# Optimization experiments

Hardware: AMD Instinct MI355X
Metric: run time of the kernel (lower is better)

## Reference

```python
import jax, jax.numpy as jnp
import numpy as np

DIM = 192
SCALE = DIM ** (-0.5)


def setup_inputs() -> dict:
    key = jax.random.key(0)
    qkv = jax.random.normal(key, (8, 4096, 3 * DIM), dtype=jnp.float32)
    return {"qkv": qkv}


def reference(qkv):
    # qkv: [B, T, 3C] -> q, k, v each [B, T, C]
    q, k, v = jnp.split(qkv, 3, axis=2)
    # scale_in=True: scale q and k before distance computation
    q = q * SCALE
    k = k * SCALE
    # L2-distance attention logits: -||q_t - k_s||_2, computed via the
    # expansion ||q||^2 + ||k||^2 - 2 q.k (same as torch.cdist for large inputs)
    q2 = jnp.sum(q * q, axis=-1)          # [B, T]
    k2 = jnp.sum(k * k, axis=-1)          # [B, S]
    d2 = q2[:, :, None] + k2[:, None, :] - 2.0 * jnp.einsum('btc,bsc->bts', q, k)
    d2 = jnp.maximum(d2, 0.0)
    # safe sqrt (zero distance on the diagonal since q and k come from same tokens)
    dist = jnp.where(d2 > 0, jnp.sqrt(jnp.where(d2 > 0, d2, 1.0)), 0.0)
    attn_logits = -dist                    # [B, T, S]
    attn = jax.nn.softmax(attn_logits, axis=-1)
    return jnp.einsum('bts,bsc->btc', attn, v)  # [B, T, C]
```

## Files before the change

### kernel.cpp

```cpp
#include <hip/hip_runtime.h>
#include <hip/hip_bf16.h>


#define BB 8
#define TT 4096
#define CD 192

typedef __attribute__((ext_vector_type(8))) short short8;
typedef __attribute__((ext_vector_type(4))) float float4v;
typedef __attribute__((ext_vector_type(2))) unsigned int uint2v;

constexpr float A2C = (float)(2.0813689810056077 / 192.0);

static __device__ __forceinline__ unsigned short f2bf(float f) {
  unsigned u = __builtin_bit_cast(unsigned, f);
  unsigned r = u + 0x7fffu + ((u >> 16) & 1u);
  return (unsigned short)(r >> 16);
}
static __device__ __forceinline__ float bf2f(unsigned short b) {
  return __builtin_bit_cast(float, (unsigned)b << 16);
}

__global__ __launch_bounds__(256) void prep(
    const float* __restrict__ qkv, short8* __restrict__ qsw,
    short8* __restrict__ ksw, short8* __restrict__ vsw,
    float* __restrict__ q2, float* __restrict__ k2) {
  __shared__ unsigned short tile[32 * 584];
  const int t = threadIdx.x;
  const int b = blockIdx.x >> 7;
  const int sc = blockIdx.x & 127;
  const float* src = qkv + ((size_t)(b * TT + sc * 32)) * (3 * CD);
#pragma unroll
  for (int j = 0; j < 18; ++j) {
    int f = j * 256 + t;
    int row = f / 144, c4 = (f % 144) * 4;
    float4v x = *(const float4v*)(src + (size_t)row * 576 + c4);
    unsigned r0 = (unsigned)f2bf(x[0]) | ((unsigned)f2bf(x[1]) << 16);
    unsigned r1 = (unsigned)f2bf(x[2]) | ((unsigned)f2bf(x[3]) << 16);
    *(uint2v*)&tile[row * 584 + c4] = (uint2v){r0, r1};
  }
  __syncthreads();

  const int lane = t & 63, w = t >> 6;
  const int L = lane & 15, q = lane >> 4;
  const int which = w >> 1;
  const int s16o = w & 1;
  const int row = s16o * 16 + L;
  short8* dst = which ? ksw : qsw;
  const size_t ubase = ((size_t)(b * 256 + sc * 2 + s16o)) * 6;
  float ss = 0.f;
#pragma unroll
  for (int ch = 0; ch < 6; ++ch) {
    short8 fr = *(const short8*)&tile[row * 584 + which * CD + ch * 32 + q * 8];
#pragma unroll
    for (int j = 0; j < 8; ++j) {
      float f = bf2f((unsigned short)fr[j]);
      ss += f * f;
    }
    dst[(ubase + ch) * 64 + lane] = fr;
  }
  ss += __shfl_xor(ss, 16);
  ss += __shfl_xor(ss, 32);
  if (lane < 16)
    (which ? k2 : q2)[b * TT + sc * 32 + s16o * 16 + lane] = ss;

#pragma unroll
  for (int i = 0; i < 3; ++i) {
    int nt2 = w * 3 + i;
    short8 fr;
#pragma unroll
    for (int j = 0; j < 8; ++j)
      fr[j] = (short)tile[(q * 8 + j) * 584 + 2 * CD + nt2 * 16 + L];
    vsw[((size_t)(b * 12 + nt2) * 128 + sc) * 64 + lane] = fr;
  }
}

__global__ __launch_bounds__(256, 1) void attn2(
    const short8* __restrict__ qsw, const short8* __restrict__ ksw,
    const short8* __restrict__ vsw, const float* __restrict__ q2,
    const float* __restrict__ k2, float* __restrict__ out) {
  __shared__ __align__(16) unsigned char s_lds[49152 + 9216];
  float* ldsP = (float*)(s_lds + 49152);

  const int tid = threadIdx.x;
  const int w = tid >> 6;
  const int lane = tid & 63;
  const int L = lane & 15;
  const int q = lane >> 4;
  const int b = blockIdx.x & 7;
  const int qt = blockIdx.x >> 3;
  const int q0 = qt * 128 + w * 32;
  const size_t bT = (size_t)b * TT;

  float* pw = ldsP + w * 576;

  auto stage = [&](int itile, int buf) {
    const char* gk = (const char*)(ksw + ((size_t)(b * 256 + 2 * itile)) * 6 * 64);
#pragma unroll
    for (int j = 0; j < 3; ++j) {
      int u = w * 3 + j;
      const char* ga = gk + (u * 64 + lane) * 16;
      char* la = (char*)s_lds + buf * 12288 + u * 1024;
      __builtin_amdgcn_global_load_lds(
          (const __attribute__((address_space(1))) void*)ga,
          (__attribute__((address_space(3))) void*)la, 16, 0, 0);
    }
#pragma unroll
    for (int j = 0; j < 3; ++j) {
      int u = w * 3 + j;
      const char* ga = (const char*)vsw +
                       (((size_t)(b * 12 + u) * 128 + itile) * 64 + lane) * 16;
      char* la = (char*)s_lds + 24576 + buf * 12288 + u * 1024;
      __builtin_amdgcn_global_load_lds(
          (const __attribute__((address_space(1))) void*)ga,
          (__attribute__((address_space(3))) void*)la, 16, 0, 0);
    }
  };

  short8 qf[2][6];
#pragma unroll
  for (int mt = 0; mt < 2; ++mt)
#pragma unroll
    for (int ch = 0; ch < 6; ++ch)
      qf[mt][ch] = qsw[((size_t)(b * 256 + (q0 >> 4) + mt) * 6 + ch) * 64 + lane];

  float q2l[2][4];
#pragma unroll
  for (int mt = 0; mt < 2; ++mt)
#pragma unroll
    for (int r = 0; r < 4; ++r)
      q2l[mt][r] = q2[bT + q0 + mt * 16 + 4 * q + r];

  float4v oacc[2][12];
#pragma unroll
  for (int mt = 0; mt < 2; ++mt)
#pragma unroll
    for (int nt = 0; nt < 12; ++nt) oacc[mt][nt] = (float4v){0.f, 0.f, 0.f, 0.f};
  float lsum[2][4] = {{0.f, 0.f, 0.f, 0.f}, {0.f, 0.f, 0.f, 0.f}};

  stage(0, 0);
  __syncthreads();

#pragma unroll 1
  for (int it = 0; it < 128; ++it) {
    const int cur = it & 1;
    if (it + 1 < 128) stage(it + 1, cur ^ 1);
    const int s0 = it * 32;

    float k2l[2];
    k2l[0] = k2[bT + s0 + L];
    k2l[1] = k2[bT + s0 + 16 + L];

    float4v sacc[2][2];
#pragma unroll
    for (int mt = 0; mt < 2; ++mt)
#pragma unroll
      for (int nt = 0; nt < 2; ++nt) sacc[mt][nt] = (float4v){0.f, 0.f, 0.f, 0.f};
#pragma unroll
    for (int ch = 0; ch < 6; ++ch) {
      short8 kf0 = *(const short8*)(s_lds + cur * 12288 + ch * 1024 + lane * 16);
      short8 kf1 = *(const short8*)(s_lds + cur * 12288 + (6 + ch) * 1024 + lane * 16);
      sacc[0][0] = __builtin_amdgcn_mfma_f32_16x16x32_bf16(qf[0][ch], kf0, sacc[0][0], 0, 0, 0);
      sacc[1][0] = __builtin_amdgcn_mfma_f32_16x16x32_bf16(qf[1][ch], kf0, sacc[1][0], 0, 0, 0);
      sacc[0][1] = __builtin_amdgcn_mfma_f32_16x16x32_bf16(qf[0][ch], kf1, sacc[0][1], 0, 0, 0);
      sacc[1][1] = __builtin_amdgcn_mfma_f32_16x16x32_bf16(qf[1][ch], kf1, sacc[1][1], 0, 0, 0);
    }

    short8 vf[12];
#pragma unroll
    for (int nt = 0; nt < 12; ++nt)
      vf[nt] = *(const short8*)(s_lds + 24576 + cur * 12288 + nt * 1024 + lane * 16);

    short8 paf[2];
#pragma unroll
    for (int mt = 0; mt < 2; ++mt) {
#pragma unroll
      for (int nt = 0; nt < 2; ++nt)
#pragma unroll
        for (int r = 0; r < 4; ++r) {
          float dot = sacc[mt][nt][r];
          float tt = fmaf(-2.f, dot, q2l[mt][r] + k2l[nt]);
          float y = fmaxf(tt, 0.f) * A2C;
          float p = __builtin_amdgcn_exp2f(-__builtin_amdgcn_sqrtf(y));
          lsum[mt][r] += p;
          pw[(4 * q + r) * 36 + nt * 16 + L] = p;
        }
      float4v p0 = *(const float4v*)(pw + L * 36 + q * 8);
      float4v p1 = *(const float4v*)(pw + L * 36 + q * 8 + 4);
      short8 pa;
#pragma unroll
      for (int j = 0; j < 4; ++j) {
        pa[j] = (short)f2bf(p0[j]);
        pa[j + 4] = (short)f2bf(p1[j]);
      }
      paf[mt] = pa;
    }

#pragma unroll
    for (int nt = 0; nt < 12; ++nt) {
      oacc[0][nt] = __builtin_amdgcn_mfma_f32_16x16x32_bf16(paf[0], vf[nt], oacc[0][nt], 0, 0, 0);
      oacc[1][nt] = __builtin_amdgcn_mfma_f32_16x16x32_bf16(paf[1], vf[nt], oacc[1][nt], 0, 0, 0);
    }

    __syncthreads();
  }

#pragma unroll
  for (int mt = 0; mt < 2; ++mt)
#pragma unroll
    for (int r = 0; r < 4; ++r) {
      float ls = lsum[mt][r];
#pragma unroll
      for (int m = 1; m < 16; m <<= 1) ls += __shfl_xor(ls, m);
      float linv = 1.f / ls;
#pragma unroll
      for (int nt = 0; nt < 12; ++nt)
        out[(bT + q0 + mt * 16 + 4 * q + r) * CD + nt * 16 + L] =
            oacc[mt][nt][r] * linv;
    }
}

extern "C" void kernel_launch(void* const* d_in, const int* in_sizes, int n_in,
                              void* d_out, int out_size, void* d_ws, size_t ws_size,
                              hipStream_t stream) {
  (void)in_sizes; (void)n_in; (void)out_size; (void)ws_size;
  const float* qkv = (const float*)d_in[0];
  float* out = (float*)d_out;

  short8* qsw = (short8*)d_ws;
  short8* ksw = qsw + (size_t)BB * 256 * 6 * 64;
  short8* vsw = ksw + (size_t)BB * 256 * 6 * 64;
  float* q2 = (float*)(vsw + (size_t)BB * 12 * 128 * 64);
  float* k2 = q2 + (size_t)BB * TT;

  prep<<<BB * 128, 256, 0, stream>>>(qkv, qsw, ksw, vsw, q2, k2);
  attn2<<<BB * 32, 256, 0, stream>>>(qsw, ksw, vsw, q2, k2, out);
}
```

Before: 303.9 us.

## Halve per-wave query rows and double grid to raise occupancy

Measured after the change: 244.3 us. -19.6%, faster.

```diff
diff --git a/kernel.cpp b/kernel.cpp
--- a/kernel.cpp
+++ b/kernel.cpp
@@ -62,7 +62,7 @@
   ss += __shfl_xor(ss, 16);
   ss += __shfl_xor(ss, 32);
   if (lane < 16)
-    (which ? k2 : q2)[b * TT + sc * 32 + s16o * 16 + lane] = ss;
+    (which ? k2 : q2)[b * TT + sc * 32 + s16o * 16 + lane] = ss * A2C;
 
 #pragma unroll
   for (int i = 0; i < 3; ++i) {
@@ -75,7 +75,7 @@
   }
 }
 
-__global__ __launch_bounds__(256, 1) void attn2(
+__global__ __launch_bounds__(256, 2) void attn2(
     const short8* __restrict__ qsw, const short8* __restrict__ ksw,
     const short8* __restrict__ vsw, const float* __restrict__ q2,
     const float* __restrict__ k2, float* __restrict__ out) {
@@ -89,7 +89,7 @@
   const int q = lane >> 4;
   const int b = blockIdx.x & 7;
   const int qt = blockIdx.x >> 3;
-  const int q0 = qt * 128 + w * 32;
+  const int q0 = qt * 64 + w * 16;
   const size_t bT = (size_t)b * TT;
 
   float* pw = ldsP + w * 576;
@@ -117,26 +117,19 @@
     }
   };
 
-  short8 qf[2][6];
-#pragma unroll
-  for (int mt = 0; mt < 2; ++mt)
-#pragma unroll
-    for (int ch = 0; ch < 6; ++ch)
-      qf[mt][ch] = qsw[((size_t)(b * 256 + (q0 >> 4) + mt) * 6 + ch) * 64 + lane];
-
-  float q2l[2][4];
-#pragma unroll
-  for (int mt = 0; mt < 2; ++mt)
-#pragma unroll
-    for (int r = 0; r < 4; ++r)
-      q2l[mt][r] = q2[bT + q0 + mt * 16 + 4 * q + r];
-
-  float4v oacc[2][12];
-#pragma unroll
-  for (int mt = 0; mt < 2; ++mt)
-#pragma unroll
-    for (int nt = 0; nt < 12; ++nt) oacc[mt][nt] = (float4v){0.f, 0.f, 0.f, 0.f};
-  float lsum[2][4] = {{0.f, 0.f, 0.f, 0.f}, {0.f, 0.f, 0.f, 0.f}};
+  short8 qf[6];
+#pragma unroll
+  for (int ch = 0; ch < 6; ++ch)
+    qf[ch] = qsw[((size_t)(b * 256 + (q0 >> 4)) * 6 + ch) * 64 + lane];
+
+  float q2l[4];
+#pragma unroll
+  for (int r = 0; r < 4; ++r) q2l[r] = q2[bT + q0 + 4 * q + r];
+
+  float4v oacc[12];
+#pragma unroll
+  for (int nt = 0; nt < 12; ++nt) oacc[nt] = (float4v){0.f, 0.f, 0.f, 0.f};
+  float lsum[4] = {0.f, 0.f, 0.f, 0.f};
 
   stage(0, 0);
   __syncthreads();
@@ -151,19 +144,15 @@
     k2l[0] = k2[bT + s0 + L];
     k2l[1] = k2[bT + s0 + 16 + L];
 
-    float4v sacc[2][2];
-#pragma unroll
-    for (int mt = 0; mt < 2; ++mt)
-#pragma unroll
-      for (int nt = 0; nt < 2; ++nt) sacc[mt][nt] = (float4v){0.f, 0.f, 0.f, 0.f};
+    float4v sacc[2];
+    sacc[0] = (float4v){0.f, 0.f, 0.f, 0.f};
+    sacc[1] = (float4v){0.f, 0.f, 0.f, 0.f};
 #pragma unroll
     for (int ch = 0; ch < 6; ++ch) {
       short8 kf0 = *(const short8*)(s_lds + cur * 12288 + ch * 1024 + lane * 16);
       short8 kf1 = *(const short8*)(s_lds + cur * 12288 + (6 + ch) * 1024 + lane * 16);
-      sacc[0][0] = __builtin_amdgcn_mfma_f32_16x16x32_bf16(qf[0][ch], kf0, sacc[0][0], 0, 0, 0);
-      sacc[1][0] = __builtin_amdgcn_mfma_f32_16x16x32_bf16(qf[1][ch], kf0, sacc[1][0], 0, 0, 0);
-      sacc[0][1] = __builtin_amdgcn_mfma_f32_16x16x32_bf16(qf[0][ch], kf1, sacc[0][1], 0, 0, 0);
-      sacc[1][1] = __builtin_amdgcn_mfma_f32_16x16x32_bf16(qf[1][ch], kf1, sacc[1][1], 0, 0, 0);
+      sacc[0] = __builtin_amdgcn_mfma_f32_16x16x32_bf16(qf[ch], kf0, sacc[0], 0, 0, 0);
+      sacc[1] = __builtin_amdgcn_mfma_f32_16x16x32_bf16(qf[ch], kf1, sacc[1], 0, 0, 0);
     }
 
     short8 vf[12];
@@ -171,53 +160,43 @@
     for (int nt = 0; nt < 12; ++nt)
       vf[nt] = *(const short8*)(s_lds + 24576 + cur * 12288 + nt * 1024 + lane * 16);
 
-    short8 paf[2];
-#pragma unroll
-    for (int mt = 0; mt < 2; ++mt) {
-#pragma unroll
-      for (int nt = 0; nt < 2; ++nt)
-#pragma unroll
-        for (int r = 0; r < 4; ++r) {
-          float dot = sacc[mt][nt][r];
-          float tt = fmaf(-2.f, dot, q2l[mt][r] + k2l[nt]);
-          float y = fmaxf(tt, 0.f) * A2C;
-          float p = __builtin_amdgcn_exp2f(-__builtin_amdgcn_sqrtf(y));
-          lsum[mt][r] += p;
-          pw[(4 * q + r) * 36 + nt * 16 + L] = p;
-        }
-      float4v p0 = *(const float4v*)(pw + L * 36 + q * 8);
-      float4v p1 = *(const float4v*)(pw + L * 36 + q * 8 + 4);
-      short8 pa;
-#pragma unroll
-      for (int j = 0; j < 4; ++j) {
-        pa[j] = (short)f2bf(p0[j]);
-        pa[j + 4] = (short)f2bf(p1[j]);
+#pragma unroll
+    for (int nt = 0; nt < 2; ++nt)
+#pragma unroll
+      for (int r = 0; r < 4; ++r) {
+        float dot = sacc[nt][r];
+        float tt = fmaf(-2.f * A2C, dot, q2l[r] + k2l[nt]);
+        float y = fmaxf(tt, 0.f);
+        float p = __builtin_amdgcn_exp2f(-__builtin_amdgcn_sqrtf(y));
+        lsum[r] += p;
+        pw[(4 * q + r) * 36 + nt * 16 + L] = p;
       }
-      paf[mt] = pa;
-    }
-
-#pragma unroll
-    for (int nt = 0; nt < 12; ++nt) {
-      oacc[0][nt] = __builtin_amdgcn_mfma_f32_16x16x32_bf16(paf[0], vf[nt], oacc[0][nt], 0, 0, 0);
-      oacc[1][nt] = __builtin_amdgcn_mfma_f32_16x16x32_bf16(paf[1], vf[nt], oacc[1][nt], 0, 0, 0);
-    }
+    float4v p0 = *(const float4v*)(pw + L * 36 + q * 8);
+    float4v p1 = *(const float4v*)(pw + L * 36 + q * 8 + 4);
+    short8 paf;
+#pragma unroll
+    for (int j = 0; j < 4; ++j) {
+      paf[j] = (short)f2bf(p0[j]);
+      paf[j + 4] = (short)f2bf(p1[j]);
+    }
+
+#pragma unroll
+    for (int nt = 0; nt < 12; ++nt)
+      oacc[nt] = __builtin_amdgcn_mfma_f32_16x16x32_bf16(paf, vf[nt], oacc[nt], 0, 0, 0);
 
     __syncthreads();
   }
 
 #pragma unroll
-  for (int mt = 0; mt < 2; ++mt)
-#pragma unroll
-    for (int r = 0; r < 4; ++r) {
-      float ls = lsum[mt][r];
-#pragma unroll
-      for (int m = 1; m < 16; m <<= 1) ls += __shfl_xor(ls, m);
-      float linv = 1.f / ls;
-#pragma unroll
-      for (int nt = 0; nt < 12; ++nt)
-        out[(bT + q0 + mt * 16 + 4 * q + r) * CD + nt * 16 + L] =
-            oacc[mt][nt][r] * linv;
-    }
+  for (int r = 0; r < 4; ++r) {
+    float ls = lsum[r];
+#pragma unroll
+    for (int m = 1; m < 16; m <<= 1) ls += __shfl_xor(ls, m);
+    float linv = 1.f / ls;
+#pragma unroll
+    for (int nt = 0; nt < 12; ++nt)
+      out[(bT + q0 + 4 * q + r) * CD + nt * 16 + L] = oacc[nt][r] * linv;
+  }
 }
 
 extern "C" void kernel_launch(void* const* d_in, const int* in_sizes, int n_in,
@@ -234,5 +213,5 @@
   float* k2 = q2 + (size_t)BB * TT;
 
   prep<<<BB * 128, 256, 0, stream>>>(qkv, qsw, ksw, vsw, q2, k2);
-  attn2<<<BB * 32, 256, 0, stream>>>(qsw, ksw, vsw, q2, k2, out);
-}
+  attn2<<<BB * 64, 256, 0, stream>>>(qsw, ksw, vsw, q2, k2, out);
+}
```
